# Optimization experiments

Measured on AMD Instinct MI355X. Metric: run time of the kernel, lower is better.

Reference implementation:

```python
import jax, jax.numpy as jnp
import numpy as np

B, C, T = 8, 512, 4096          # batch, channels (query/key/value/calc), time
NUM_HEADS = 8
HEAD_DIM = C // NUM_HEADS
EPS = 1e-6


def _rmsnorm(x, g):
    # x: [B, C, T], normalize over channel dim (num_features)
    return x * jax.lax.rsqrt(jnp.mean(x * x, axis=1, keepdims=True) + EPS) * g[None, :, None]


def _conv1x1(x, W, b):
    # pointwise Conv1d: W [out, in], x [B, in, T]
    return jnp.einsum('oc,bct->bot', W, x) + b[None, :, None]


def _feature(x, W, b, g):
    # Conv1d -> RMSNorm -> elu(x)+1
    return jax.nn.elu(_rmsnorm(_conv1x1(x, W, b), g)) + 1.0


def setup_inputs() -> dict:
    key = jax.random.key(0)
    ks = jax.random.split(key, 16)
    s = 1.0 / np.sqrt(C)
    inp = {
        'queries': jax.random.normal(ks[0], (B, C, T), dtype=jnp.float32),
        'keys': jax.random.normal(ks[1], (B, C, T), dtype=jnp.float32),
        'values': jax.random.normal(ks[2], (B, C, T), dtype=jnp.float32),
        'key_padding_masks': jax.random.randint(ks[3], (B, T), 0, 2).astype(bool),
        'Wq': jax.random.normal(ks[4], (C, C), dtype=jnp.float32) * s,
        'bq': jnp.zeros((C,), dtype=jnp.float32),
        'gq': jnp.ones((C,), dtype=jnp.float32),
        'Wk': jax.random.normal(ks[5], (C, C), dtype=jnp.float32) * s,
        'bk': jnp.zeros((C,), dtype=jnp.float32),
        'gk': jnp.ones((C,), dtype=jnp.float32),
        'Wv': jax.random.normal(ks[6], (C, C), dtype=jnp.float32) * s,
        'bv': jnp.zeros((C,), dtype=jnp.float32),
        'gv': jnp.ones((C,), dtype=jnp.float32),
        'Wp': jax.random.normal(ks[7], (C, C), dtype=jnp.float32) * s,
        'bp': jnp.zeros((C,), dtype=jnp.float32),
        'g_out': jnp.ones((C,), dtype=jnp.float32),
    }
    return inp


def reference(queries, keys, values, key_padding_masks,
              Wq, bq, gq, Wk, bk, gk, Wv, bv, gv, Wp, bp, g_out):
    residuals = queries
    q = _feature(queries, Wq, bq, gq)   # [B, C, Tq]
    k = _feature(keys, Wk, bk, gk)      # [B, C, Tk]
    v = _feature(values, Wv, bv, gv)    # [B, C, Tk]

    # split heads: (head dim) channel layout -> [B, H, Dh, T]
    q = q.reshape(B, NUM_HEADS, HEAD_DIM, -1)
    k = k.reshape(B, NUM_HEADS, HEAD_DIM, -1)
    v = v.reshape(B, NUM_HEADS, HEAD_DIM, -1)

    k = jnp.where(key_padding_masks[:, None, None, :], -10000.0, k)

    q = jax.nn.softmax(q, axis=2) * (NUM_HEADS ** -0.5)  # softmax over head_dim
    k = jax.nn.softmax(k, axis=3)                         # softmax over key time
    v = v / HEAD_DIM

    # linear attention: KV composition then QKV
    ctx = jnp.einsum('bhkt,bhvt->bhkv', k, v)             # [B, H, Dh, Dh]
    out = jnp.einsum('bhqt,bhqv->bhvt', q, ctx)           # [B, H, Dh, Tq]

    out = out.reshape(B, C, -1)
    out = _conv1x1(out, Wp, bp)
    return _rmsnorm(out + residuals, g_out)
```

## Files before the change

kernel.cpp:

```cpp
#include <hip/hip_runtime.h>
#include <hip/hip_bf16.h>

#define BB 8
#define CC 512
#define TT 4096
#define HH 8
#define DH 64
#define EPS 1e-6f

#define NROWS (BB * TT)

using bf16x8 = __attribute__((ext_vector_type(8))) short;
using s16x4  = __attribute__((ext_vector_type(4))) short;
using f32x4  = __attribute__((ext_vector_type(4))) float;

__device__ __forceinline__ short f2b(float f) {
  __hip_bfloat16 h = __float2bfloat16(f);
  return *reinterpret_cast<short*>(&h);
}
__device__ __forceinline__ float b2f(short s) {
  unsigned u = ((unsigned)(unsigned short)s) << 16;
  return __uint_as_float(u);
}

__device__ __forceinline__ void gld16(short* lds_dst, const short* gsrc) {
  __builtin_amdgcn_global_load_lds(
      (const __attribute__((address_space(1))) unsigned int*)gsrc,
      (__attribute__((address_space(3))) unsigned int*)lds_dst, 16, 0, 0);
}

__global__ __launch_bounds__(256) void conv_w4(const float* __restrict__ s0, const float* __restrict__ s1,
                                               const float* __restrict__ s2, const float* __restrict__ s3,
                                               short* __restrict__ d0, short* __restrict__ d1,
                                               short* __restrict__ d2, short* __restrict__ d3)
{
  const float* src; short* dst;
  switch (blockIdx.y) {
    case 0: src = s0; dst = d0; break;
    case 1: src = s1; dst = d1; break;
    case 2: src = s2; dst = d2; break;
    default: src = s3; dst = d3; break;
  }
  int i8 = (blockIdx.x * 256 + threadIdx.x) * 8;
  float4 a = *(const float4*)(src + i8);
  float4 b = *(const float4*)(src + i8 + 4);
  bf16x8 h = { f2b(a.x), f2b(a.y), f2b(a.z), f2b(a.w),
               f2b(b.x), f2b(b.y), f2b(b.z), f2b(b.w) };
  *(bf16x8*)(dst + i8) = h;
}

#define TSTR 120
__device__ __forceinline__ int tadr(int c, int t) {
  return c * TSTR + ((c >> 3) & 7) * 8 + t;
}

__global__ __launch_bounds__(256) void transpose_cvt3(const float* __restrict__ X0,
                                                      const float* __restrict__ X1,
                                                      const float* __restrict__ X2,
                                                      short* __restrict__ Y0,
                                                      short* __restrict__ Y1,
                                                      short* __restrict__ Y2)
{
  __shared__ short tile[64 * TSTR];
  const int t0 = blockIdx.x * 256, c0 = blockIdx.y * 64;
  const int b = blockIdx.z & 7, which = blockIdx.z >> 3;
  const float* X = which == 0 ? X0 : (which == 1 ? X1 : X2);
  short* Xt = which == 0 ? Y0 : (which == 1 ? Y1 : Y2);
  const int tid = threadIdx.x;
  const int cl = tid >> 4, t4 = (tid & 15) * 4;
  const int T2 = (tid >> 3) * 2, ci = (tid & 7) * 8;

  float4 rc[4];
  #pragma unroll
  for (int it = 0; it < 4; ++it)
    rc[it] = *(const float4*)(X + ((size_t)b * CC + c0 + it * 16 + cl) * TT + t0 + t4);

  #pragma unroll
  for (int s = 0; s < 4; ++s) {
    float4 rn[4];
    if (s < 3) {
      #pragma unroll
      for (int it = 0; it < 4; ++it)
        rn[it] = *(const float4*)(X + ((size_t)b * CC + c0 + it * 16 + cl) * TT
                                  + t0 + (s + 1) * 64 + t4);
    }
    #pragma unroll
    for (int it = 0; it < 4; ++it) {
      s16x4 h = { f2b(rc[it].x), f2b(rc[it].y), f2b(rc[it].z), f2b(rc[it].w) };
      *(s16x4*)&tile[tadr(it * 16 + cl, t4)] = h;
    }
    asm volatile("s_waitcnt lgkmcnt(0)" ::: "memory");
    __builtin_amdgcn_s_barrier();
    __builtin_amdgcn_sched_barrier(0);
    unsigned u[8];
    #pragma unroll
    for (int i = 0; i < 8; ++i)
      u[i] = *(const unsigned*)&tile[tadr(ci + i, T2)];
    short lo[8], hi[8];
    #pragma unroll
    for (int i = 0; i < 8; ++i) {
      lo[i] = (short)(u[i] & 0xffffu);
      hi[i] = (short)(u[i] >> 16);
    }
    short* dst0 = Xt + ((size_t)b * TT + t0 + s * 64 + T2) * CC + c0 + ci;
    *(bf16x8*)dst0 = *(bf16x8*)&lo[0];
    *(bf16x8*)(dst0 + CC) = *(bf16x8*)&hi[0];
    __builtin_amdgcn_sched_barrier(0);
    __builtin_amdgcn_s_barrier();
    __builtin_amdgcn_sched_barrier(0);
    #pragma unroll
    for (int it = 0; it < 4; ++it) rc[it] = rn[it];
  }
}

__device__ __forceinline__ void gemm_body(const short* __restrict__ A,
                                          const short* __restrict__ W,
                                          const float* __restrict__ bias,
                                          short* __restrict__ Y,
                                          short* As, short* Bs, int x, int tid)
{
  int wg = (x & 7) * 128 + (x >> 3);
  const int m0 = (wg >> 2) * 128;
  const int o0 = (wg & 3) * 128;

  const int wid = tid >> 6, lane = tid & 63;
  const int wr = (wid >> 1) * 64, wc = (wid & 1) * 64;
  const int lr = lane & 15, g = lane >> 4;
  const int swz8 = (g ^ ((lr >> 1) & 3)) * 8;

  const int srow0 = tid >> 2;
  const int scol  = ((tid & 3) ^ ((tid >> 3) & 3)) * 8;

  f32x4 acc[4][4] = {};

  #pragma unroll
  for (int it = 0; it < 2; ++it) {
    int row = it * 64 + srow0;
    gld16(&As[it * 2048 + tid * 8], A + (size_t)(m0 + row) * CC + scol);
    gld16(&Bs[it * 2048 + tid * 8], W + (size_t)(o0 + row) * CC + scol);
  }

  for (int step = 0; step < 16; ++step) {
    const int cur = step & 1;
    if (step < 15) {
      const int k0 = (step + 1) * 32;
      #pragma unroll
      for (int it = 0; it < 2; ++it) {
        int row = it * 64 + srow0;
        gld16(&As[(cur ^ 1) * 4096 + it * 2048 + tid * 8], A + (size_t)(m0 + row) * CC + k0 + scol);
        gld16(&Bs[(cur ^ 1) * 4096 + it * 2048 + tid * 8], W + (size_t)(o0 + row) * CC + k0 + scol);
      }
      asm volatile("s_waitcnt vmcnt(4)" ::: "memory");
    } else {
      asm volatile("s_waitcnt vmcnt(0)" ::: "memory");
    }
    __builtin_amdgcn_s_barrier();
    __builtin_amdgcn_sched_barrier(0);

    bf16x8 af[4], bf[4];
    #pragma unroll
    for (int m = 0; m < 4; ++m) af[m] = *(const bf16x8*)&As[cur * 4096 + (wr + m * 16 + lr) * 32 + swz8];
    #pragma unroll
    for (int n = 0; n < 4; ++n) bf[n] = *(const bf16x8*)&Bs[cur * 4096 + (wc + n * 16 + lr) * 32 + swz8];
    #pragma unroll
    for (int m = 0; m < 4; ++m)
      #pragma unroll
      for (int n = 0; n < 4; ++n)
        acc[m][n] = __builtin_amdgcn_mfma_f32_16x16x32_bf16(af[m], bf[n], acc[m][n], 0, 0, 0);

    __builtin_amdgcn_sched_barrier(0);
    __builtin_amdgcn_s_barrier();
    __builtin_amdgcn_sched_barrier(0);
  }

  const int lq4 = (lane >> 4) * 4;
  #pragma unroll
  for (int m = 0; m < 4; ++m)
    #pragma unroll
    for (int r = 0; r < 4; ++r) {
      size_t row = (size_t)(m0 + wr + m * 16 + lq4 + r) * CC;
      #pragma unroll
      for (int n = 0; n < 4; ++n) {
        int o = o0 + wc + n * 16 + lr;
        Y[row + o] = f2b(acc[m][n][r] + bias[o]);
      }
    }
}

__global__ __launch_bounds__(256) void gemm_tc3(
    const short* __restrict__ A0, const short* __restrict__ A1, const short* __restrict__ A2,
    const short* __restrict__ W0, const short* __restrict__ W1, const short* __restrict__ W2,
    const float* __restrict__ b0, const float* __restrict__ b1, const float* __restrict__ b2,
    short* __restrict__ Y0, short* __restrict__ Y1, short* __restrict__ Y2)
{
  __shared__ short As[2 * 4096];
  __shared__ short Bs[2 * 4096];
  const short *A, *W; const float* bias; short* Y;
  switch (blockIdx.y) {
    case 0:  A = A0; W = W0; bias = b0; Y = Y0; break;
    case 1:  A = A1; W = W1; bias = b1; Y = Y1; break;
    default: A = A2; W = W2; bias = b2; Y = Y2; break;
  }
  gemm_body(A, W, bias, Y, As, Bs, blockIdx.x, threadIdx.x);
}

__global__ __launch_bounds__(256) void gemm_tc(const short* __restrict__ A,
                                               const short* __restrict__ W,
                                               const float* __restrict__ bias,
                                               short* __restrict__ Y)
{
  __shared__ short As[2 * 4096];
  __shared__ short Bs[2 * 4096];
  gemm_body(A, W, bias, Y, As, Bs, blockIdx.x, threadIdx.x);
}

__global__ __launch_bounds__(256) void feat_all(short* __restrict__ qf, short* __restrict__ kf,
                                                short* __restrict__ vf,
                                                const float* __restrict__ gq,
                                                const float* __restrict__ gk,
                                                const float* __restrict__ gv,
                                                const unsigned char* __restrict__ mask)
{
  const int mode = blockIdx.y;
  short* buf = mode == 0 ? qf : (mode == 1 ? kf : vf);
  const float* g = mode == 0 ? gq : (mode == 1 ? gk : gv);
  const int row = blockIdx.x * 4 + (threadIdx.x >> 6);
  const int lane = threadIdx.x & 63;
  short* p = buf + (size_t)row * CC + lane * 8;
  if (mode == 1 && mask[row]) {
    bf16x8 z = { 0,0,0,0,0,0,0,0 };
    *(bf16x8*)p = z;
    return;
  }
  bf16x8 v = *(const bf16x8*)p;
  float x[8], ss = 0.f;
  #pragma unroll
  for (int j = 0; j < 8; ++j) { x[j] = b2f(v[j]); ss += x[j] * x[j]; }
  #pragma unroll
  for (int off = 32; off; off >>= 1) ss += __shfl_xor(ss, off);
  float rn = rsqrtf(ss * (1.0f / CC) + EPS);
  float4 g0 = *(const float4*)(g + lane * 8);
  float4 g1 = *(const float4*)(g + lane * 8 + 4);
  float gv8[8] = { g0.x, g0.y, g0.z, g0.w, g1.x, g1.y, g1.z, g1.w };
  float f[8];
  #pragma unroll
  for (int j = 0; j < 8; ++j) {
    float t = x[j] * rn * gv8[j];
    f[j] = t > 0.f ? t + 1.f : __expf(t);
  }
  bf16x8 o;
  if (mode == 1) {
    #pragma unroll
    for (int j = 0; j < 8; ++j) o[j] = f2b(__expf(f[j]));
  } else if (mode == 2) {
    #pragma unroll
    for (int j = 0; j < 8; ++j) o[j] = f2b(f[j] * (1.0f / DH));
  } else {
    float ls = 0.f;
    #pragma unroll
    for (int j = 0; j < 8; ++j) { f[j] = __expf(f[j]); ls += f[j]; }
    ls += __shfl_xor(ls, 1); ls += __shfl_xor(ls, 2); ls += __shfl_xor(ls, 4);
    float sc = 0.35355339059327373f / ls;
    #pragma unroll
    for (int j = 0; j < 8; ++j) o[j] = f2b(f[j] * sc);
  }
  *(bf16x8*)p = o;
}

__global__ __launch_bounds__(256) void ksm_sum(const short* __restrict__ kfe,
                                               float* __restrict__ S)
{
  const int b = blockIdx.y, tch = blockIdx.x;
  const int c2 = threadIdx.x * 2;
  float s0 = 0.f, s1 = 0.f;
  for (int t = 0; t < 128; ++t) {
    unsigned u = *(const unsigned*)&kfe[((size_t)b * TT + tch * 128 + t) * CC + c2];
    s0 += __uint_as_float(u << 16);
    s1 += __uint_as_float(u & 0xffff0000u);
  }
  atomicAdd(&S[b * CC + c2], s0);
  atomicAdd(&S[b * CC + c2 + 1], s1);
}

__global__ __launch_bounds__(256) void ctx_t(const short* __restrict__ kf,
                                             const short* __restrict__ vf,
                                             float* __restrict__ P)
{
  __shared__ short Ks[64 * 64];
  __shared__ short Vs[64 * 64];
  const int tc = blockIdx.x, bh = blockIdx.y;
  const int b = bh >> 3, h = bh & 7;
  const int tid = threadIdx.x, wid = tid >> 6, lane = tid & 63;
  const int lr = lane & 15, lg = lane >> 4;
  f32x4 acc[4] = {};

  for (int ts = 0; ts < 8; ++ts) {
    #pragma unroll
    for (int i = 0; i < 2; ++i) {
      int n = i * 256 + tid;
      int t = n >> 3, ch = (n & 7) * 8;
      size_t src = ((size_t)b * TT + tc * 512 + ts * 64 + t) * CC + h * DH + ch;
      gld16(Ks + n * 8, kf + src);
      gld16(Vs + n * 8, vf + src);
    }
    __syncthreads();
    #pragma unroll
    for (int kk = 0; kk < 64; kk += 32) {
      short a[8];
      #pragma unroll
      for (int j = 0; j < 8; ++j)
        a[j] = Ks[(kk + lg * 8 + j) * 64 + wid * 16 + lr];
      bf16x8 af = *(const bf16x8*)&a[0];
      #pragma unroll
      for (int n = 0; n < 4; ++n) {
        short bv[8];
        #pragma unroll
        for (int j = 0; j < 8; ++j)
          bv[j] = Vs[(kk + lg * 8 + j) * 64 + n * 16 + lr];
        acc[n] = __builtin_amdgcn_mfma_f32_16x16x32_bf16(af, *(const bf16x8*)&bv[0],
                                                         acc[n], 0, 0, 0);
      }
    }
    __syncthreads();
  }
  float* pp = P + ((size_t)tc * 64 + bh) * (DH * DH);
  const int lq4 = lg * 4;
  #pragma unroll
  for (int n = 0; n < 4; ++n)
    #pragma unroll
    for (int r = 0; r < 4; ++r)
      pp[(wid * 16 + lq4 + r) * DH + n * 16 + lr] = acc[n][r];
}

__global__ __launch_bounds__(256) void ctx_reduce(const float* __restrict__ P,
                                                  const float* __restrict__ S,
                                                  short* __restrict__ CT)
{
  int i = blockIdx.x * 256 + threadIdx.x;
  float s = 0.f;
  #pragma unroll
  for (int c = 0; c < 8; ++c) s += P[(size_t)c * 64 * DH * DH + i];
  int bh = i >> 12, rem = i & 4095, q = rem >> 6, v = rem & 63;
  int b = bh >> 3, h = bh & 7;
  float inv = 1.f / S[b * CC + h * DH + q];
  CT[((size_t)bh << 12) + v * 64 + q] = f2b(s * inv);
}

__global__ __launch_bounds__(256) void attn_t(const short* __restrict__ qf,
                                              const short* __restrict__ CT,
                                              short* __restrict__ ao)
{
  __shared__ short As[128 * 72];
  __shared__ short Cs[64 * 72];
  const int m0 = blockIdx.x * 128, h = blockIdx.y;
  const int tid = threadIdx.x, wid = tid >> 6, lane = tid & 63;
  const int lr = lane & 15, lk8 = (lane >> 4) * 8;

  #pragma unroll
  for (int i = 0; i < 4; ++i) {
    int n = i * 256 + tid;
    int r = n >> 3, ch = (n & 7) * 8;
    *(bf16x8*)&As[r * 72 + ch] =
        *(const bf16x8*)(qf + (size_t)(m0 + r) * CC + h * DH + ch);
  }
  {
    const int bh0 = (m0 / TT) * 8 + h;
    #pragma unroll
    for (int i = 0; i < 2; ++i) {
      int n = i * 256 + tid;
      int v = n >> 3, ch = (n & 7) * 8;
      *(bf16x8*)&Cs[v * 72 + ch] = *(const bf16x8*)(CT + ((size_t)bh0 << 12) + v * 64 + ch);
    }
  }
  __syncthreads();

  const int wr = wid * 32;
  f32x4 acc[2][4] = {};
  #pragma unroll
  for (int kk = 0; kk < 64; kk += 32) {
    bf16x8 af[2], cf[4];
    #pragma unroll
    for (int m = 0; m < 2; ++m) af[m] = *(const bf16x8*)&As[(wr + m * 16 + lr) * 72 + kk + lk8];
    #pragma unroll
    for (int n = 0; n < 4; ++n) cf[n] = *(const bf16x8*)&Cs[(n * 16 + lr) * 72 + kk + lk8];
    #pragma unroll
    for (int m = 0; m < 2; ++m)
      #pragma unroll
      for (int n = 0; n < 4; ++n)
        acc[m][n] = __builtin_amdgcn_mfma_f32_16x16x32_bf16(af[m], cf[n], acc[m][n], 0, 0, 0);
  }
  const int lq4 = (lane >> 4) * 4;
  #pragma unroll
  for (int m = 0; m < 2; ++m)
    #pragma unroll
    for (int r = 0; r < 4; ++r) {
      size_t row = (size_t)(m0 + wr + m * 16 + lq4 + r) * CC + h * DH;
      #pragma unroll
      for (int n = 0; n < 4; ++n)
        ao[row + n * 16 + lr] = f2b(acc[m][n][r]);
    }
}

__global__ __launch_bounds__(256) void final_fused(const short* __restrict__ pj,
                                                   const short* __restrict__ qt,
                                                   const float* __restrict__ g,
                                                   float* __restrict__ out)
{
  __shared__ short z[512 * 72];
  __shared__ float rmss[64];
  const int t0 = blockIdx.x * 64, b = blockIdx.y;
  const int tid = threadIdx.x;

  {
    const int t = tid >> 2, cb = (tid & 3) * 128;
    const size_t row = ((size_t)b * TT + t0 + t) * CC + cb;
    float ss = 0.f;
    #pragma unroll
    for (int j = 0; j < 16; ++j) {
      bf16x8 a = *(const bf16x8*)(pj + row + j * 8);
      bf16x8 q = *(const bf16x8*)(qt + row + j * 8);
      #pragma unroll
      for (int e = 0; e < 8; ++e) {
        float zf = b2f(a[e]) + b2f(q[e]);
        ss += zf * zf;
        z[(cb + j * 8 + e) * 72 + t] = f2b(zf);
      }
    }
    ss += __shfl_xor(ss, 1);
    ss += __shfl_xor(ss, 2);
    if ((tid & 3) == 0) rmss[t] = rsqrtf(ss * (1.0f / CC) + EPS);
  }
  __syncthreads();

  const int c = tid >> 2, tcs = (tid & 3) * 16;
  #pragma unroll 1
  for (int cb8 = 0; cb8 < 8; ++cb8) {
    const int cc = cb8 * 64 + c;
    const float gc = g[cc];
    bf16x8 z0 = *(const bf16x8*)&z[cc * 72 + tcs];
    bf16x8 z1 = *(const bf16x8*)&z[cc * 72 + tcs + 8];
    float* dst = out + ((size_t)b * CC + cc) * TT + t0 + tcs;
    #pragma unroll
    for (int i = 0; i < 2; ++i) {
      float4 o0 = { b2f(z0[i*4+0]) * rmss[tcs+i*4+0] * gc, b2f(z0[i*4+1]) * rmss[tcs+i*4+1] * gc,
                    b2f(z0[i*4+2]) * rmss[tcs+i*4+2] * gc, b2f(z0[i*4+3]) * rmss[tcs+i*4+3] * gc };
      *(float4*)(dst + i * 4) = o0;
    }
    #pragma unroll
    for (int i = 0; i < 2; ++i) {
      float4 o1 = { b2f(z1[i*4+0]) * rmss[tcs+8+i*4+0] * gc, b2f(z1[i*4+1]) * rmss[tcs+8+i*4+1] * gc,
                    b2f(z1[i*4+2]) * rmss[tcs+8+i*4+2] * gc, b2f(z1[i*4+3]) * rmss[tcs+8+i*4+3] * gc };
      *(float4*)(dst + 8 + i * 4) = o1;
    }
  }
}

extern "C" void kernel_launch(void* const* d_in, const int* in_sizes, int n_in,
                              void* d_out, int out_size, void* d_ws, size_t ws_size,
                              hipStream_t stream) {
  (void)in_sizes; (void)n_in; (void)out_size; (void)ws_size;
  const float* queries = (const float*)d_in[0];
  const float* keys    = (const float*)d_in[1];
  const float* values  = (const float*)d_in[2];
  const unsigned char* mask = (const unsigned char*)d_in[3];
  const float* Wq = (const float*)d_in[4];
  const float* bq = (const float*)d_in[5];
  const float* gq = (const float*)d_in[6];
  const float* Wk = (const float*)d_in[7];
  const float* bk = (const float*)d_in[8];
  const float* gk = (const float*)d_in[9];
  const float* Wv = (const float*)d_in[10];
  const float* bv = (const float*)d_in[11];
  const float* gv = (const float*)d_in[12];
  const float* Wp = (const float*)d_in[13];
  const float* bp = (const float*)d_in[14];
  const float* g_out = (const float*)d_in[15];

  const size_t NCT = (size_t)NROWS * CC;
  short* qt = (short*)d_ws;
  short* kt = qt + NCT;
  short* vt = kt + NCT;
  short* qf = vt + NCT;
  short* kf = qf + NCT;
  short* vf = kf + NCT;
  short* ao = kt;
  short* pj = vt;
  float* ctxP = (float*)(vf + NCT);
  short* CT  = (short*)(ctxP + (size_t)8 * 64 * DH * DH);
  short* wqb = CT + (size_t)64 * DH * DH;
  short* wkb = wqb + (size_t)CC * CC;
  short* wvb = wkb + (size_t)CC * CC;
  short* wpb = wvb + (size_t)CC * CC;
  float* S   = (float*)(wpb + (size_t)CC * CC);

  hipMemsetAsync(S, 0, (size_t)BB * CC * sizeof(float), stream);

  conv_w4<<<dim3(CC * CC / 2048, 4), 256, 0, stream>>>(Wq, Wk, Wv, Wp, wqb, wkb, wvb, wpb);

  transpose_cvt3<<<dim3(TT / 256, CC / 64, 3 * BB), 256, 0, stream>>>(
      queries, keys, values, qt, kt, vt);

  gemm_tc3<<<dim3(1024, 3), 256, 0, stream>>>(qt, kt, vt, wqb, wkb, wvb,
                                              bq, bk, bv, qf, kf, vf);

  feat_all<<<dim3(NROWS / 4, 3), 256, 0, stream>>>(qf, kf, vf, gq, gk, gv, mask);

  ksm_sum<<<dim3(32, BB), 256, 0, stream>>>(kf, S);

  ctx_t<<<dim3(8, BB * HH), 256, 0, stream>>>(kf, vf, ctxP);
  ctx_reduce<<<dim3(64 * DH * DH / 256), 256, 0, stream>>>(ctxP, S, CT);

  attn_t<<<dim3(NROWS / 128, HH), 256, 0, stream>>>(qf, CT, ao);

  gemm_tc<<<dim3(1024), 256, 0, stream>>>(ao, wpb, bp, pj);

  final_fused<<<dim3(TT / 64, BB), 256, 0, stream>>>(pj, qt, g_out, (float*)d_out);
}
```

Baseline: 320.6 us.

## Fuse QKV projection GEMM with RMSNorm, feature map and key-sum epilogue

Replaces the three-way projection GEMM, the separate feature kernel and the key column-sum kernel with one kernel. Each 512-thread block computes a full 128-row by 512-column output tile, so the per-row RMS norm, elu+1, softmax exponentials and masking run in the epilogue from registers, and the key sums are added to S with atomics. This removes a bf16 write and re-read of the three projected tensors plus two launches. In exchange the block holds 128 accumulator floats per thread and a larger weight tile in LDS, which can lower occupancy, and the output stores are scattered 2-byte writes.

```diff
diff --git a/kernel.cpp b/kernel.cpp
--- a/kernel.cpp
+++ b/kernel.cpp
@@ -113,12 +113,191 @@
   }
 }
 
-__device__ __forceinline__ void gemm_body(const short* __restrict__ A,
-                                          const short* __restrict__ W,
-                                          const float* __restrict__ bias,
-                                          short* __restrict__ Y,
-                                          short* As, short* Bs, int x, int tid)
-{
+__global__ __launch_bounds__(512, 2) void gemm_feat3(
+    const short* __restrict__ qt, const short* __restrict__ kt, const short* __restrict__ vt,
+    const short* __restrict__ wq, const short* __restrict__ wk, const short* __restrict__ wv,
+    const float* __restrict__ bq, const float* __restrict__ bk, const float* __restrict__ bv,
+    const float* __restrict__ gq, const float* __restrict__ gk, const float* __restrict__ gv,
+    const unsigned char* __restrict__ mask, float* __restrict__ S,
+    short* __restrict__ qf, short* __restrict__ kf, short* __restrict__ vf)
+{
+  __shared__ short As[2][128 * 32];
+  __shared__ short Ws[2][512 * 32];
+  const int mode = blockIdx.y;
+  const short* A = mode == 0 ? qt : (mode == 1 ? kt : vt);
+  const short* W = mode == 0 ? wq : (mode == 1 ? wk : wv);
+  const float* bias = mode == 0 ? bq : (mode == 1 ? bk : bv);
+  const float* g = mode == 0 ? gq : (mode == 1 ? gk : gv);
+  short* Y = mode == 0 ? qf : (mode == 1 ? kf : vf);
+
+  const int m0 = blockIdx.x * 128;
+  const int tid = threadIdx.x;
+  const int w = tid >> 6, lane = tid & 63;
+  const int lr = lane & 15, lg = lane >> 4;
+  const int swz8 = (lg ^ ((lr >> 1) & 3)) * 8;
+  const int arow = tid >> 2, ach = tid & 3;
+  const int ascol = (ach ^ ((arow >> 1) & 3)) * 8;
+
+  f32x4 acc[8][4] = {};
+
+  gld16(&As[0][tid * 8], A + (size_t)(m0 + arow) * CC + ascol);
+  #pragma unroll
+  for (int it = 0; it < 4; ++it) {
+    int slot = it * 512 + tid;
+    int wrow = slot >> 2, wch = slot & 3;
+    gld16(&Ws[0][slot * 8], W + (size_t)wrow * CC + ((wch ^ ((wrow >> 1) & 3)) * 8));
+  }
+
+  for (int step = 0; step < 16; ++step) {
+    const int cur = step & 1;
+    if (step < 15) {
+      const int k0 = (step + 1) * 32;
+      gld16(&As[cur ^ 1][tid * 8], A + (size_t)(m0 + arow) * CC + k0 + ascol);
+      #pragma unroll
+      for (int it = 0; it < 4; ++it) {
+        int slot = it * 512 + tid;
+        int wrow = slot >> 2, wch = slot & 3;
+        gld16(&Ws[cur ^ 1][slot * 8], W + (size_t)wrow * CC + k0 + ((wch ^ ((wrow >> 1) & 3)) * 8));
+      }
+      asm volatile("s_waitcnt vmcnt(5)" ::: "memory");
+    } else {
+      asm volatile("s_waitcnt vmcnt(0)" ::: "memory");
+    }
+    __builtin_amdgcn_s_barrier();
+    __builtin_amdgcn_sched_barrier(0);
+
+    bf16x8 af[8];
+    #pragma unroll
+    for (int mf = 0; mf < 8; ++mf)
+      af[mf] = *(const bf16x8*)&As[cur][(mf * 16 + lr) * 32 + swz8];
+    #pragma unroll
+    for (int nf = 0; nf < 4; ++nf) {
+      bf16x8 bfv = *(const bf16x8*)&Ws[cur][(w * 64 + nf * 16 + lr) * 32 + swz8];
+      #pragma unroll
+      for (int mf = 0; mf < 8; ++mf)
+        acc[mf][nf] = __builtin_amdgcn_mfma_f32_16x16x32_bf16(af[mf], bfv, acc[mf][nf], 0, 0, 0);
+    }
+    __builtin_amdgcn_sched_barrier(0);
+    __builtin_amdgcn_s_barrier();
+    __builtin_amdgcn_sched_barrier(0);
+  }
+
+  float* ssb  = (float*)&As[0][0];
+  float* rmsb = ssb + 1024;
+  const int b = m0 >> 12;
+
+  float bcol[4], gcol[4];
+  #pragma unroll
+  for (int nf = 0; nf < 4; ++nf) {
+    int col = w * 64 + nf * 16 + lr;
+    bcol[nf] = bias[col];
+    gcol[nf] = g[col];
+  }
+
+  #pragma unroll
+  for (int mf = 0; mf < 8; ++mf) {
+    #pragma unroll
+    for (int r = 0; r < 4; ++r) {
+      float p = 0.f;
+      #pragma unroll
+      for (int nf = 0; nf < 4; ++nf) {
+        float v = acc[mf][nf][r] + bcol[nf];
+        acc[mf][nf][r] = v;
+        p += v * v;
+      }
+      p += __shfl_xor(p, 1); p += __shfl_xor(p, 2);
+      p += __shfl_xor(p, 4); p += __shfl_xor(p, 8);
+      if (lr == 0) ssb[w * 128 + mf * 16 + lg * 4 + r] = p;
+    }
+  }
+  __syncthreads();
+  if (tid < 128) {
+    float tot = 0.f;
+    #pragma unroll
+    for (int ww = 0; ww < 8; ++ww) tot += ssb[ww * 128 + tid];
+    rmsb[tid] = rsqrtf(tot * (1.0f / CC) + EPS);
+  }
+  __syncthreads();
+
+  if (mode == 2) {
+    #pragma unroll
+    for (int mf = 0; mf < 8; ++mf)
+      #pragma unroll
+      for (int r = 0; r < 4; ++r) {
+        int rl = mf * 16 + lg * 4 + r;
+        float rn = rmsb[rl];
+        size_t rowoff = (size_t)(m0 + rl) * CC;
+        #pragma unroll
+        for (int nf = 0; nf < 4; ++nf) {
+          float x = acc[mf][nf][r] * rn * gcol[nf];
+          float f = x > 0.f ? x + 1.f : __expf(x);
+          Y[rowoff + w * 64 + nf * 16 + lr] = f2b(f * (1.0f / DH));
+        }
+      }
+  } else if (mode == 1) {
+    float ks[4] = { 0.f, 0.f, 0.f, 0.f };
+    #pragma unroll
+    for (int mf = 0; mf < 8; ++mf)
+      #pragma unroll
+      for (int r = 0; r < 4; ++r) {
+        int rl = mf * 16 + lg * 4 + r;
+        float rn = rmsb[rl];
+        bool mk = mask[m0 + rl] != 0;
+        size_t rowoff = (size_t)(m0 + rl) * CC;
+        #pragma unroll
+        for (int nf = 0; nf < 4; ++nf) {
+          float x = acc[mf][nf][r] * rn * gcol[nf];
+          float f = x > 0.f ? x + 1.f : __expf(x);
+          float e = mk ? 0.f : __expf(f);
+          ks[nf] += e;
+          Y[rowoff + w * 64 + nf * 16 + lr] = f2b(e);
+        }
+      }
+    #pragma unroll
+    for (int nf = 0; nf < 4; ++nf) {
+      ks[nf] += __shfl_xor(ks[nf], 16);
+      ks[nf] += __shfl_xor(ks[nf], 32);
+    }
+    if (lane < 16) {
+      #pragma unroll
+      for (int nf = 0; nf < 4; ++nf)
+        atomicAdd(&S[b * CC + w * 64 + nf * 16 + lr], ks[nf]);
+    }
+  } else {
+    #pragma unroll
+    for (int mf = 0; mf < 8; ++mf)
+      #pragma unroll
+      for (int r = 0; r < 4; ++r) {
+        int rl = mf * 16 + lg * 4 + r;
+        float rn = rmsb[rl];
+        float es[4]; float qs = 0.f;
+        #pragma unroll
+        for (int nf = 0; nf < 4; ++nf) {
+          float x = acc[mf][nf][r] * rn * gcol[nf];
+          float f = x > 0.f ? x + 1.f : __expf(x);
+          float e = __expf(f);
+          es[nf] = e; qs += e;
+        }
+        qs += __shfl_xor(qs, 1); qs += __shfl_xor(qs, 2);
+        qs += __shfl_xor(qs, 4); qs += __shfl_xor(qs, 8);
+        float sc = 0.35355339059327373f / qs;
+        size_t rowoff = (size_t)(m0 + rl) * CC;
+        #pragma unroll
+        for (int nf = 0; nf < 4; ++nf)
+          Y[rowoff + w * 64 + nf * 16 + lr] = f2b(es[nf] * sc);
+      }
+  }
+}
+
+__global__ __launch_bounds__(256) void gemm_tc(const short* __restrict__ A,
+                                               const short* __restrict__ W,
+                                               const float* __restrict__ bias,
+                                               short* __restrict__ Y)
+{
+  __shared__ short As[2 * 4096];
+  __shared__ short Bs[2 * 4096];
+  const int tid = threadIdx.x;
+  int x = blockIdx.x;
   int wg = (x & 7) * 128 + (x >> 3);
   const int m0 = (wg >> 2) * 128;
   const int o0 = (wg & 3) * 128;
@@ -127,7 +306,6 @@
   const int wr = (wid >> 1) * 64, wc = (wid & 1) * 64;
   const int lr = lane & 15, g = lane >> 4;
   const int swz8 = (g ^ ((lr >> 1) & 3)) * 8;
-
   const int srow0 = tid >> 2;
   const int scol  = ((tid & 3) ^ ((tid >> 3) & 3)) * 8;
 
@@ -185,101 +363,6 @@
         Y[row + o] = f2b(acc[m][n][r] + bias[o]);
       }
     }
-}
-
-__global__ __launch_bounds__(256) void gemm_tc3(
-    const short* __restrict__ A0, const short* __restrict__ A1, const short* __restrict__ A2,
-    const short* __restrict__ W0, const short* __restrict__ W1, const short* __restrict__ W2,
-    const float* __restrict__ b0, const float* __restrict__ b1, const float* __restrict__ b2,
-    short* __restrict__ Y0, short* __restrict__ Y1, short* __restrict__ Y2)
-{
-  __shared__ short As[2 * 4096];
-  __shared__ short Bs[2 * 4096];
-  const short *A, *W; const float* bias; short* Y;
-  switch (blockIdx.y) {
-    case 0:  A = A0; W = W0; bias = b0; Y = Y0; break;
-    case 1:  A = A1; W = W1; bias = b1; Y = Y1; break;
-    default: A = A2; W = W2; bias = b2; Y = Y2; break;
-  }
-  gemm_body(A, W, bias, Y, As, Bs, blockIdx.x, threadIdx.x);
-}
-
-__global__ __launch_bounds__(256) void gemm_tc(const short* __restrict__ A,
-                                               const short* __restrict__ W,
-                                               const float* __restrict__ bias,
-                                               short* __restrict__ Y)
-{
-  __shared__ short As[2 * 4096];
-  __shared__ short Bs[2 * 4096];
-  gemm_body(A, W, bias, Y, As, Bs, blockIdx.x, threadIdx.x);
-}
-
-__global__ __launch_bounds__(256) void feat_all(short* __restrict__ qf, short* __restrict__ kf,
-                                                short* __restrict__ vf,
-                                                const float* __restrict__ gq,
-                                                const float* __restrict__ gk,
-                                                const float* __restrict__ gv,
-                                                const unsigned char* __restrict__ mask)
-{
-  const int mode = blockIdx.y;
-  short* buf = mode == 0 ? qf : (mode == 1 ? kf : vf);
-  const float* g = mode == 0 ? gq : (mode == 1 ? gk : gv);
-  const int row = blockIdx.x * 4 + (threadIdx.x >> 6);
-  const int lane = threadIdx.x & 63;
-  short* p = buf + (size_t)row * CC + lane * 8;
-  if (mode == 1 && mask[row]) {
-    bf16x8 z = { 0,0,0,0,0,0,0,0 };
-    *(bf16x8*)p = z;
-    return;
-  }
-  bf16x8 v = *(const bf16x8*)p;
-  float x[8], ss = 0.f;
-  #pragma unroll
-  for (int j = 0; j < 8; ++j) { x[j] = b2f(v[j]); ss += x[j] * x[j]; }
-  #pragma unroll
-  for (int off = 32; off; off >>= 1) ss += __shfl_xor(ss, off);
-  float rn = rsqrtf(ss * (1.0f / CC) + EPS);
-  float4 g0 = *(const float4*)(g + lane * 8);
-  float4 g1 = *(const float4*)(g + lane * 8 + 4);
-  float gv8[8] = { g0.x, g0.y, g0.z, g0.w, g1.x, g1.y, g1.z, g1.w };
-  float f[8];
-  #pragma unroll
-  for (int j = 0; j < 8; ++j) {
-    float t = x[j] * rn * gv8[j];
-    f[j] = t > 0.f ? t + 1.f : __expf(t);
-  }
-  bf16x8 o;
-  if (mode == 1) {
-    #pragma unroll
-    for (int j = 0; j < 8; ++j) o[j] = f2b(__expf(f[j]));
-  } else if (mode == 2) {
-    #pragma unroll
-    for (int j = 0; j < 8; ++j) o[j] = f2b(f[j] * (1.0f / DH));
-  } else {
-    float ls = 0.f;
-    #pragma unroll
-    for (int j = 0; j < 8; ++j) { f[j] = __expf(f[j]); ls += f[j]; }
-    ls += __shfl_xor(ls, 1); ls += __shfl_xor(ls, 2); ls += __shfl_xor(ls, 4);
-    float sc = 0.35355339059327373f / ls;
-    #pragma unroll
-    for (int j = 0; j < 8; ++j) o[j] = f2b(f[j] * sc);
-  }
-  *(bf16x8*)p = o;
-}
-
-__global__ __launch_bounds__(256) void ksm_sum(const short* __restrict__ kfe,
-                                               float* __restrict__ S)
-{
-  const int b = blockIdx.y, tch = blockIdx.x;
-  const int c2 = threadIdx.x * 2;
-  float s0 = 0.f, s1 = 0.f;
-  for (int t = 0; t < 128; ++t) {
-    unsigned u = *(const unsigned*)&kfe[((size_t)b * TT + tch * 128 + t) * CC + c2];
-    s0 += __uint_as_float(u << 16);
-    s1 += __uint_as_float(u & 0xffff0000u);
-  }
-  atomicAdd(&S[b * CC + c2], s0);
-  atomicAdd(&S[b * CC + c2 + 1], s1);
 }
 
 __global__ __launch_bounds__(256) void ctx_t(const short* __restrict__ kf,
@@ -500,12 +583,8 @@
   transpose_cvt3<<<dim3(TT / 256, CC / 64, 3 * BB), 256, 0, stream>>>(
       queries, keys, values, qt, kt, vt);
 
-  gemm_tc3<<<dim3(1024, 3), 256, 0, stream>>>(qt, kt, vt, wqb, wkb, wvb,
-                                              bq, bk, bv, qf, kf, vf);
-
-  feat_all<<<dim3(NROWS / 4, 3), 256, 0, stream>>>(qf, kf, vf, gq, gk, gv, mask);
-
-  ksm_sum<<<dim3(32, BB), 256, 0, stream>>>(kf, S);
+  gemm_feat3<<<dim3(NROWS / 128, 3), 512, 0, stream>>>(
+      qt, kt, vt, wqb, wkb, wvb, bq, bk, bv, gq, gk, gv, mask, S, qf, kf, vf);
 
   ctx_t<<<dim3(8, BB * HH), 256, 0, stream>>>(kf, vf, ctxP);
   ctx_reduce<<<dim3(64 * DH * DH / 256), 256, 0, stream>>>(ctxP, S, CT);
```

Result: slower. 334.6 us (+4.4%).
